# Optimization experiments

Hardware: AMD Instinct MI355X
Metric: run time of the kernel (lower is better)

Reference implementation:

```python
import jax, jax.numpy as jnp
import numpy as np

S, N, CM, CZ, H, D = 512, 768, 64, 128, 8, 32
EPS = 1e-5


def _layer_norm(x, w, b):
    mu = jnp.mean(x, axis=-1, keepdims=True)
    xc = x - mu
    var = jnp.mean(xc * xc, axis=-1, keepdims=True)
    return xc * jax.lax.rsqrt(var + EPS) * w + b


def setup_inputs() -> dict:
    key = jax.random.key(0)
    ks = jax.random.split(key, 6)
    scale_m = 1.0 / np.sqrt(CM)
    scale_z = 1.0 / np.sqrt(CZ)
    scale_o = 1.0 / np.sqrt(H * D)
    return {
        "m": jax.random.normal(ks[0], (1, S, N, CM), jnp.float32),
        "z": jax.random.normal(ks[1], (1, N, N, CZ), jnp.float32),
        "norm_m_w": jnp.ones((CM,), jnp.float32),
        "norm_m_b": jnp.zeros((CM,), jnp.float32),
        "norm_z_w": jnp.ones((CZ,), jnp.float32),
        "norm_z_b": jnp.zeros((CZ,), jnp.float32),
        "wm": jax.random.normal(ks[2], (CM, H * D), jnp.float32) * scale_m,
        "wg": jax.random.normal(ks[3], (CM, H * D), jnp.float32) * scale_m,
        "wz": jax.random.normal(ks[4], (CZ, H), jnp.float32) * scale_z,
        "wo": jax.random.normal(ks[5], (H * D, CM), jnp.float32) * scale_o,
    }


def reference(m, z, norm_m_w, norm_m_b, norm_z_w, norm_z_b, wm, wg, wz, wo):
    m0 = m[0]  # [S, N, CM]
    z0 = z[0]  # [N, N, CZ]
    mn = _layer_norm(m0, norm_m_w, norm_m_b)
    zn = _layer_norm(z0, norm_z_w, norm_z_b)
    # b[p,q,h]; original code softmaxes over the LAST axis of b'[h,p,q] (axis q)
    # but contracts as o[s,q] = sum_p w[p,q] v[s,p] (transpose_a matmul),
    # so softmax is over axis q = axis 1 of [p,q,h].
    b = jnp.einsum('pqc,ch->pqh', zn, wz)
    w = jax.nn.softmax(b, axis=1)  # normalized over q for each p (faithful to source)
    v = jnp.einsum('spc,ck->spk', mn, wm).reshape(S, N, H, D)
    g = jax.nn.sigmoid(jnp.einsum('spc,ck->spk', mn, wg)).reshape(S, N, H, D)
    o = jnp.einsum('pqh,sphd->sqhd', w, v) * g  # weighted average then gate
    out = jnp.einsum('sqhd,hdc->sqc', o, wo.reshape(H, D, CM))
    return out[None]  # [1, S, N, CM]
```

## Files before the change

kernel.cpp:

```cpp
#include <hip/hip_runtime.h>
#include <hip/hip_bf16.h>
#include <stdint.h>

#define S_DIM 512
#define N_DIM 768
#define CMd   64
#define CZd   128
#define Hd    8
#define Dd    32
#define HDd   256

typedef float          f32x4  __attribute__((ext_vector_type(4)));
typedef __bf16         bf16x8 __attribute__((ext_vector_type(8)));
typedef unsigned int   u32x4  __attribute__((ext_vector_type(4)));
typedef unsigned int   u32x2  __attribute__((ext_vector_type(2)));
typedef unsigned short u16x8  __attribute__((ext_vector_type(8)));

__device__ __forceinline__ unsigned short f2bf(float f) {
  __bf16 h = (__bf16)f;
  return __builtin_bit_cast(unsigned short, h);
}
__device__ __forceinline__ float bf2f(unsigned short u) {
  unsigned int x = ((unsigned int)u) << 16;
  return __builtin_bit_cast(float, x);
}
__device__ __forceinline__ float sigmoidf_(float x) {
  return 1.f / (1.f + __expf(-x));
}

typedef __attribute__((address_space(1))) const void cg_void;
typedef __attribute__((address_space(3))) void lds_void;
__device__ __forceinline__ void async16(const unsigned short* g, unsigned short* l) {
  __builtin_amdgcn_global_load_lds((cg_void*)g, (lds_void*)l, 16, 0, 0);
}

__global__ __launch_bounds__(256) void k0_prep(const float* __restrict__ wm,
                                               const float* __restrict__ wg,
                                               const float* __restrict__ wo,
                                               unsigned short* __restrict__ WBT,
                                               unsigned short* __restrict__ woT) {
  int t = blockIdx.x * 256 + threadIdx.x;
  if (t < 512 * 64) {
    int j = t >> 6, c = t & 63;
    float v = (j < 256) ? wm[c * 256 + j] : wg[c * 256 + (j - 256)];
    WBT[t] = f2bf(v);
  }
  if (t < 64 * 256) {
    int c = t >> 8, k = t & 255;
    woT[t] = f2bf(wo[k * 64 + c]);
  }
}

__global__ __launch_bounds__(256) void k1_zln_b(const float* __restrict__ z,
                                                const float* __restrict__ nzw,
                                                const float* __restrict__ nzb,
                                                const float* __restrict__ wz,
                                                float* __restrict__ b_e) {
  __shared__ float wzT[8][128];
  int t = threadIdx.x;
  for (int i = t; i < 1024; i += 256) {
    int h = i >> 7, c = i & 127;
    wzT[h][c] = wz[c * 8 + h];
  }
  __syncthreads();

  int lane = t & 63, w = t >> 6;
  int sub = lane & 7;
  int rloc = lane >> 3;
  int p = blockIdx.y;
  int q = blockIdx.x * 32 + w * 8 + rloc;

  const float* zr = z + ((size_t)p * N_DIM + q) * CZd + sub * 16;
  f32x4 v[4];
#pragma unroll
  for (int j = 0; j < 4; j++) v[j] = *(const f32x4*)(zr + 4 * j);

  float s1 = 0.f, s2 = 0.f;
#pragma unroll
  for (int j = 0; j < 4; j++)
#pragma unroll
    for (int e = 0; e < 4; e++) { float x = v[j][e]; s1 += x; s2 += x * x; }
  s1 += __shfl_xor(s1, 1); s2 += __shfl_xor(s2, 1);
  s1 += __shfl_xor(s1, 2); s2 += __shfl_xor(s2, 2);
  s1 += __shfl_xor(s1, 4); s2 += __shfl_xor(s2, 4);
  float mean = s1 * (1.f / 128.f);
  float var  = s2 * (1.f / 128.f) - mean * mean;
  float rstd = rsqrtf(var + 1e-5f);

  const float* wp = nzw + sub * 16;
  const float* bp = nzb + sub * 16;
  float zn[16];
#pragma unroll
  for (int j = 0; j < 4; j++) {
    f32x4 wv = *(const f32x4*)(wp + 4 * j);
    f32x4 bv = *(const f32x4*)(bp + 4 * j);
#pragma unroll
    for (int e = 0; e < 4; e++)
      zn[j * 4 + e] = (v[j][e] - mean) * rstd * wv[e] + bv[e];
  }

  float accb[8];
#pragma unroll
  for (int h = 0; h < 8; h++) {
    const f32x4* wr = (const f32x4*)&wzT[h][sub * 16];
    float a = 0.f;
#pragma unroll
    for (int j = 0; j < 4; j++) {
      f32x4 ww = wr[j];
#pragma unroll
      for (int e = 0; e < 4; e++) a += zn[j * 4 + e] * ww[e];
    }
    accb[h] = a;
  }
#pragma unroll
  for (int mask = 1; mask <= 4; mask <<= 1)
#pragma unroll
    for (int h = 0; h < 8; h++) accb[h] += __shfl_xor(accb[h], mask);

  float outv = accb[0];
#pragma unroll
  for (int h = 1; h < 8; h++) outv = (sub == h) ? accb[h] : outv;
  b_e[((size_t)p * 8 + sub) * 768 + q] = outv;
}

__global__ __launch_bounds__(256) void k1b_softmax(float* __restrict__ b_e,
                                                   float* __restrict__ invs) {
  int row = blockIdx.x;
  int t = threadIdx.x;
  float* base = b_e + (size_t)row * 768;
  float x0 = base[t], x1 = base[t + 256], x2 = base[t + 512];
  __shared__ float red[256];
  red[t] = fmaxf(x0, fmaxf(x1, x2));
  __syncthreads();
  for (int o = 128; o > 0; o >>= 1) {
    if (t < o) red[t] = fmaxf(red[t], red[t + o]);
    __syncthreads();
  }
  float M = red[0];
  __syncthreads();
  float e0 = __expf(x0 - M), e1 = __expf(x1 - M), e2 = __expf(x2 - M);
  base[t] = e0; base[t + 256] = e1; base[t + 512] = e2;
  red[t] = e0 + e1 + e2;
  __syncthreads();
  for (int o = 128; o > 0; o >>= 1) {
    if (t < o) red[t] += red[t + o];
    __syncthreads();
  }
  if (t == 0) invs[row] = 1.0f / red[0];
}

__global__ __launch_bounds__(256) void k1b2_transpose(const float* __restrict__ b_e,
                                                      const float* __restrict__ invs,
                                                      unsigned short* __restrict__ Aw) {
  int t = threadIdx.x;
  int q0 = blockIdx.x * 64, p0 = blockIdx.y * 64, h = blockIdx.z;
  __shared__ unsigned short T[64][65];
  int i = t >> 2, ch = t & 3;
  size_t rowid = (size_t)(p0 + i) * 8 + h;
  const float* src = b_e + rowid * 768 + q0 + ch * 16;
  float inv = invs[rowid];
#pragma unroll
  for (int jj = 0; jj < 16; jj += 4) {
    f32x4 v = *(const f32x4*)(src + jj);
#pragma unroll
    for (int e = 0; e < 4; e++) T[i][ch * 16 + jj + e] = f2bf(v[e] * inv);
  }
  __syncthreads();
  int j = i;
  unsigned short outv[16];
#pragma unroll
  for (int ii = 0; ii < 16; ii++) outv[ii] = T[ch * 16 + ii][j];
  int rx = (j & 7) << 3;
  unsigned short* dstrow = Aw + ((size_t)h * 768 + q0 + j) * 768 + p0;
  *(u32x4*)(dstrow + ((ch * 16) ^ rx))     = *(u32x4*)(outv);
  *(u32x4*)(dstrow + ((ch * 16 + 8) ^ rx)) = *(u32x4*)(outv + 8);
}

__global__ __launch_bounds__(256) void k2_mln_vg(const float* __restrict__ mp,
                                                 const float* __restrict__ nmw,
                                                 const float* __restrict__ nmb,
                                                 const unsigned short* __restrict__ WBT,
                                                 unsigned short* __restrict__ VT,
                                                 unsigned short* __restrict__ G) {
  __shared__ unsigned short WBs[512 * 64];
  __shared__ unsigned short As[64 * 64];
  int t = threadIdx.x;
  int p0 = blockIdx.x * 64, s = blockIdx.y;

#pragma unroll
  for (int it = 0; it < 16; it++) {
    int cid = t + it * 256;
    int row = cid >> 3, ch = cid & 7;
    u32x4 v = *(const u32x4*)(WBT + row * 64 + ch * 8);
    *(u32x4*)(WBs + row * 64 + ((ch * 8) ^ ((row & 7) << 3))) = v;
  }

  {
    int row = t >> 2, qt = t & 3;
    const float* mr = mp + ((size_t)s * N_DIM + p0 + row) * CMd + qt * 16;
    f32x4 v[4];
#pragma unroll
    for (int j = 0; j < 4; j++) v[j] = *(const f32x4*)(mr + 4 * j);
    float s1 = 0.f, s2 = 0.f;
#pragma unroll
    for (int j = 0; j < 4; j++)
#pragma unroll
      for (int e = 0; e < 4; e++) { float x = v[j][e]; s1 += x; s2 += x * x; }
    s1 += __shfl_xor(s1, 1); s2 += __shfl_xor(s2, 1);
    s1 += __shfl_xor(s1, 2); s2 += __shfl_xor(s2, 2);
    float mean = s1 * (1.f / 64.f);
    float var  = s2 * (1.f / 64.f) - mean * mean;
    float rstd = rsqrtf(var + 1e-5f);
    unsigned short o[16];
#pragma unroll
    for (int j = 0; j < 4; j++) {
      f32x4 wv = *(const f32x4*)(nmw + qt * 16 + 4 * j);
      f32x4 bv = *(const f32x4*)(nmb + qt * 16 + 4 * j);
#pragma unroll
      for (int e = 0; e < 4; e++)
        o[j * 4 + e] = f2bf((v[j][e] - mean) * rstd * wv[e] + bv[e]);
    }
    int k0 = qt * 16;
    *(u32x4*)(As + row * 64 + ((k0) ^ ((row & 7) << 3)))     = *(u32x4*)(o);
    *(u32x4*)(As + row * 64 + ((k0 + 8) ^ ((row & 7) << 3))) = *(u32x4*)(o + 8);
  }
  __syncthreads();

  int lane = t & 63, w = t >> 6;
  int n0 = w * 128;
  int lr = lane & 15, lg = lane >> 4, lk8 = lg * 8;
  f32x4 zero = {0.f, 0.f, 0.f, 0.f};
  f32x4 acc[4][8];
#pragma unroll
  for (int i = 0; i < 4; i++)
#pragma unroll
    for (int j = 0; j < 8; j++) acc[i][j] = zero;

#pragma unroll
  for (int kk = 0; kk < 2; kk++) {
    bf16x8 bfr[8];
#pragma unroll
    for (int nt = 0; nt < 8; nt++) {
      int r = n0 + nt * 16 + lr;
      bfr[nt] = *(const bf16x8*)(WBs + r * 64 + ((kk * 32 + lk8) ^ ((r & 7) << 3)));
    }
#pragma unroll
    for (int mt = 0; mt < 4; mt++) {
      int ar = mt * 16 + lr;
      bf16x8 a = *(const bf16x8*)(As + ar * 64 + ((kk * 32 + lk8) ^ ((ar & 7) << 3)));
#pragma unroll
      for (int nt = 0; nt < 8; nt++)
        acc[mt][nt] = __builtin_amdgcn_mfma_f32_16x16x32_bf16(a, bfr[nt], acc[mt][nt], 0, 0, 0);
    }
  }

  __syncthreads();

  {
    unsigned short* VL = WBs;
    if (w < 2) {
#pragma unroll
      for (int mt = 0; mt < 4; mt++)
#pragma unroll
        for (int nt = 0; nt < 8; nt++) {
          int j = n0 + nt * 16 + lr;
          int ploc = mt * 16 + lg * 4;
          unsigned short pk[4];
#pragma unroll
          for (int r = 0; r < 4; r++) pk[r] = f2bf(acc[mt][nt][r]);
          *(u32x2*)(VL + j * 72 + ploc) = *(u32x2*)pk;
        }
    }
    __syncthreads();
    int h = t >> 5, d = t & 31;
    unsigned short* dst = VT + ((size_t)h * 16384 + s * 32 + d) * 768 + p0;
    const unsigned short* src = VL + t * 72;
#pragma unroll
    for (int i = 0; i < 8; i++) {
      u32x4 v = *(const u32x4*)(src + i * 8);
      *(u32x4*)(dst + ((i ^ (d & 7)) * 8)) = v;
    }
  }
  __syncthreads();

  {
    unsigned short* GL = WBs;
    if (w >= 2) {
#pragma unroll
      for (int mt = 0; mt < 4; mt++)
#pragma unroll
        for (int nt = 0; nt < 8; nt++) {
          int jj = n0 - 256 + nt * 16 + lr;
          int ploc = mt * 16 + lg * 4;
#pragma unroll
          for (int r = 0; r < 4; r++)
            GL[(ploc + r) * 264 + jj] = f2bf(sigmoidf_(acc[mt][nt][r]));
        }
    }
    __syncthreads();
    int qrow = t >> 2, part = t & 3;
    unsigned short* dst = G + ((size_t)s * 768 + p0 + qrow) * 256 + part * 64;
    const unsigned short* src = GL + qrow * 264 + part * 64;
#pragma unroll
    for (int i = 0; i < 8; i++)
      *(u32x4*)(dst + i * 8) = *(const u32x4*)(src + i * 8);
  }
}

__global__ __launch_bounds__(256) void k3_gemm(const unsigned short* __restrict__ Aw,
                                               const unsigned short* __restrict__ VT,
                                               unsigned short* __restrict__ O) {
  __shared__ unsigned short Asl[128 * 64];
  __shared__ unsigned short Bsl[128 * 64];
  int t = threadIdx.x;
  int flat = blockIdx.x;
  int h = blockIdx.y;
  int f2 = (flat & 7) * 96 + (flat >> 3);
  int mt_b = f2 % 6, nt_b = f2 / 6;
  int q0 = mt_b * 128, n0 = nt_b * 128;

  const unsigned short* Ab = Aw + (size_t)h * 768 * 768 + (size_t)q0 * 768;
  const unsigned short* Bb = VT + (size_t)h * 16384 * 768 + (size_t)n0 * 768;

  int lane = t & 63, w = t >> 6;
  int wr = (w >> 1) * 64, wc = (w & 1) * 64;
  int lr = lane & 15;

  const unsigned short* gA = Ab + (size_t)(w * 32 + (lane >> 3)) * 768 + (lane & 7) * 8;
  const unsigned short* gB = Bb + (size_t)(w * 32 + (lane >> 3)) * 768 + (lane & 7) * 8;
  unsigned short* lA = Asl + w * 2048;
  unsigned short* lB = Bsl + w * 2048;

  f32x4 zero = {0.f, 0.f, 0.f, 0.f};
  f32x4 acc[4][4];
#pragma unroll
  for (int i = 0; i < 4; i++)
#pragma unroll
    for (int j = 0; j < 4; j++) acc[i][j] = zero;

  for (int kt = 0; kt < 12; kt++) {
    int ko = kt * 64;
#pragma unroll
    for (int i = 0; i < 4; i++) {
      async16(gA + (size_t)i * 8 * 768 + ko, lA + i * 512);
      async16(gB + (size_t)i * 8 * 768 + ko, lB + i * 512);
    }
    asm volatile("s_waitcnt vmcnt(0)" ::: "memory");
    __builtin_amdgcn_sched_barrier(0);
    __syncthreads();
#pragma unroll
    for (int kk = 0; kk < 2; kk++) {
      int kc = kk * 32 + (lane >> 4) * 8;
      bf16x8 afr[4], bfr[4];
#pragma unroll
      for (int i = 0; i < 4; i++) {
        int arr = wr + i * 16 + lr;
        int brr = wc + i * 16 + lr;
        afr[i] = *(const bf16x8*)(Asl + arr * 64 + (kc ^ ((arr & 7) << 3)));
        bfr[i] = *(const bf16x8*)(Bsl + brr * 64 + (kc ^ ((brr & 7) << 3)));
      }
#pragma unroll
      for (int mt = 0; mt < 4; mt++)
#pragma unroll
        for (int nt = 0; nt < 4; nt++)
          acc[mt][nt] = __builtin_amdgcn_mfma_f32_16x16x32_bf16(afr[mt], bfr[nt], acc[mt][nt], 0, 0, 0);
    }
    __syncthreads();
  }

#pragma unroll
  for (int mt = 0; mt < 4; mt++)
#pragma unroll
    for (int nt = 0; nt < 4; nt++) {
      int q = q0 + wr + mt * 16 + (lane >> 4) * 4;
      int n = n0 + wc + nt * 16 + lr;
      int s_ = n >> 5, d = n & 31;
      size_t ob = ((size_t)s_ * 768 + q) * 256 + h * 32 + d;
#pragma unroll
      for (int r = 0; r < 4; r++)
        O[ob + (size_t)r * 256] = f2bf(acc[mt][nt][r]);
    }
}

__global__ __launch_bounds__(256) void k4_out(const unsigned short* __restrict__ O,
                                              const unsigned short* __restrict__ G,
                                              const unsigned short* __restrict__ woT,
                                              float* __restrict__ out) {
  __shared__ unsigned short OGs[64 * 256];
  __shared__ unsigned short WOs[64 * 256];
  int t = threadIdx.x;
  int q0 = blockIdx.x * 64, s = blockIdx.y;

#pragma unroll
  for (int it = 0; it < 8; it++) {
    int cid = t + it * 256;
    int row = cid >> 5, ch = cid & 31;
    u32x4 v = *(const u32x4*)(woT + row * 256 + ch * 8);
    *(u32x4*)(WOs + row * 256 + ((ch * 8) ^ ((row & 7) << 3))) = v;
  }

  int i = t >> 2, c4 = t & 3;
  const unsigned short* Orow = O + ((size_t)s * 768 + q0 + i) * 256 + c4 * 64;
  const unsigned short* Grow = G + ((size_t)s * 768 + q0 + i) * 256 + c4 * 64;
#pragma unroll
  for (int jj = 0; jj < 8; jj++) {
    u16x8 ov = *(const u16x8*)(Orow + jj * 8);
    u16x8 gv = *(const u16x8*)(Grow + jj * 8);
    unsigned short pk[8];
#pragma unroll
    for (int e = 0; e < 8; e++) pk[e] = f2bf(bf2f(ov[e]) * bf2f(gv[e]));
    *(u32x4*)(OGs + i * 256 + ((c4 * 64 + jj * 8) ^ ((i & 7) << 3))) = *(u32x4*)pk;
  }
  __syncthreads();

  int lane = t & 63, w = t >> 6;
  int lr = lane & 15, lk8 = (lane >> 4) * 8;
  f32x4 zero = {0.f, 0.f, 0.f, 0.f};
  f32x4 acc[4];
#pragma unroll
  for (int nt = 0; nt < 4; nt++) acc[nt] = zero;

#pragma unroll
  for (int kk = 0; kk < 8; kk++) {
    int ar = w * 16 + lr;
    bf16x8 a = *(const bf16x8*)(OGs + ar * 256 + ((kk * 32 + lk8) ^ ((ar & 7) << 3)));
#pragma unroll
    for (int nt = 0; nt < 4; nt++) {
      int br = nt * 16 + lr;
      bf16x8 b = *(const bf16x8*)(WOs + br * 256 + ((kk * 32 + lk8) ^ ((br & 7) << 3)));
      acc[nt] = __builtin_amdgcn_mfma_f32_16x16x32_bf16(a, b, acc[nt], 0, 0, 0);
    }
  }

#pragma unroll
  for (int nt = 0; nt < 4; nt++) {
    int q = q0 + w * 16 + (lane >> 4) * 4;
    int c = nt * 16 + lr;
    float* dst = out + ((size_t)s * 768 + q) * 64 + c;
#pragma unroll
    for (int r = 0; r < 4; r++) dst[(size_t)r * 64] = acc[nt][r];
  }
}

extern "C" void kernel_launch(void* const* d_in, const int* in_sizes, int n_in,
                              void* d_out, int out_size, void* d_ws, size_t ws_size,
                              hipStream_t stream) {
  const float* m   = (const float*)d_in[0];
  const float* z   = (const float*)d_in[1];
  const float* nmw = (const float*)d_in[2];
  const float* nmb = (const float*)d_in[3];
  const float* nzw = (const float*)d_in[4];
  const float* nzb = (const float*)d_in[5];
  const float* wm  = (const float*)d_in[6];
  const float* wg  = (const float*)d_in[7];
  const float* wz  = (const float*)d_in[8];
  const float* wo  = (const float*)d_in[9];
  float* out = (float*)d_out;

  char* ws = (char*)d_ws;
  size_t off = 0;
  auto alloc = [&](size_t bytes) -> void* {
    void* p = ws + off;
    off += (bytes + 1023) & ~(size_t)1023;
    return p;
  };
  float*          b_e  = (float*)alloc((size_t)768 * 8 * 768 * 4);
  float*          invs = (float*)alloc((size_t)768 * 8 * 4);
  unsigned short* Awt  = (unsigned short*)alloc((size_t)8 * 768 * 768 * 2);
  unsigned short* WBT  = (unsigned short*)alloc((size_t)512 * 64 * 2);
  unsigned short* woT  = (unsigned short*)alloc((size_t)64 * 256 * 2);
  unsigned short* VT   = (unsigned short*)alloc((size_t)8 * 16384 * 768 * 2);
  unsigned short* G    = (unsigned short*)alloc((size_t)512 * 768 * 256 * 2);
  unsigned short* O    = (unsigned short*)alloc((size_t)512 * 768 * 256 * 2);
  if (ws_size < off) return;

  k0_prep<<<128, 256, 0, stream>>>(wm, wg, wo, WBT, woT);
  k1_zln_b<<<dim3(24, 768), 256, 0, stream>>>(z, nzw, nzb, wz, b_e);
  k1b_softmax<<<6144, 256, 0, stream>>>(b_e, invs);
  k1b2_transpose<<<dim3(12, 12, 8), 256, 0, stream>>>(b_e, invs, Awt);
  k2_mln_vg<<<dim3(12, 512), 256, 0, stream>>>(m, nmw, nmb, WBT, VT, G);
  k3_gemm<<<dim3(768, 8), 256, 0, stream>>>(Awt, VT, O);
  k4_out<<<dim3(12, 512), 256, 0, stream>>>(O, G, woT, out);
}
```

Baseline: 725.0 us.

## Split V/G projection across grid z and fuse gating into GEMM epilogue

The m-projection kernel is split into two grid halves, one computing V and one computing the sigmoid gate G. Weights are loaded straight from global memory into registers instead of a 64KB LDS copy, which cuts LDS use and allows a higher occupancy bound. The layer norm of m is now computed twice. The gate multiply moves from the output kernel into the k3 GEMM epilogue. That epilogue now reads G with a strided per-element pattern, while k4 no longer reads G at all.

```diff
diff --git a/kernel.cpp b/kernel.cpp
--- a/kernel.cpp
+++ b/kernel.cpp
@@ -176,24 +176,27 @@
   *(u32x4*)(dstrow + ((ch * 16 + 8) ^ rx)) = *(u32x4*)(outv + 8);
 }
 
-__global__ __launch_bounds__(256) void k2_mln_vg(const float* __restrict__ mp,
-                                                 const float* __restrict__ nmw,
-                                                 const float* __restrict__ nmb,
-                                                 const unsigned short* __restrict__ WBT,
-                                                 unsigned short* __restrict__ VT,
-                                                 unsigned short* __restrict__ G) {
-  __shared__ unsigned short WBs[512 * 64];
+__global__ __launch_bounds__(256, 3) void k2_mln_vg(const float* __restrict__ mp,
+                                                    const float* __restrict__ nmw,
+                                                    const float* __restrict__ nmb,
+                                                    const unsigned short* __restrict__ WBT,
+                                                    unsigned short* __restrict__ VT,
+                                                    unsigned short* __restrict__ G) {
   __shared__ unsigned short As[64 * 64];
-  int t = threadIdx.x;
-  int p0 = blockIdx.x * 64, s = blockIdx.y;
-
-#pragma unroll
-  for (int it = 0; it < 16; it++) {
-    int cid = t + it * 256;
-    int row = cid >> 3, ch = cid & 7;
-    u32x4 v = *(const u32x4*)(WBT + row * 64 + ch * 8);
-    *(u32x4*)(WBs + row * 64 + ((ch * 8) ^ ((row & 7) << 3))) = v;
-  }
+  __shared__ unsigned short TB[256 * 72];
+  int t = threadIdx.x;
+  int p0 = blockIdx.x * 64, s = blockIdx.y, nh = blockIdx.z;
+  int lane = t & 63, w = t >> 6;
+  int lr = lane & 15, lg = lane >> 4;
+
+  bf16x8 bfr[2][4];
+#pragma unroll
+  for (int kk = 0; kk < 2; kk++)
+#pragma unroll
+    for (int nt = 0; nt < 4; nt++) {
+      int j = nh * 256 + w * 64 + nt * 16 + lr;
+      bfr[kk][nt] = *(const bf16x8*)(WBT + j * 64 + kk * 32 + lg * 8);
+    }
 
   {
     int row = t >> 2, qt = t & 3;
@@ -226,81 +229,64 @@
   }
   __syncthreads();
 
-  int lane = t & 63, w = t >> 6;
-  int n0 = w * 128;
-  int lr = lane & 15, lg = lane >> 4, lk8 = lg * 8;
   f32x4 zero = {0.f, 0.f, 0.f, 0.f};
-  f32x4 acc[4][8];
+  f32x4 acc[4][4];
 #pragma unroll
   for (int i = 0; i < 4; i++)
 #pragma unroll
-    for (int j = 0; j < 8; j++) acc[i][j] = zero;
+    for (int j = 0; j < 4; j++) acc[i][j] = zero;
 
 #pragma unroll
   for (int kk = 0; kk < 2; kk++) {
-    bf16x8 bfr[8];
-#pragma unroll
-    for (int nt = 0; nt < 8; nt++) {
-      int r = n0 + nt * 16 + lr;
-      bfr[nt] = *(const bf16x8*)(WBs + r * 64 + ((kk * 32 + lk8) ^ ((r & 7) << 3)));
-    }
+    bf16x8 afr[4];
 #pragma unroll
     for (int mt = 0; mt < 4; mt++) {
       int ar = mt * 16 + lr;
-      bf16x8 a = *(const bf16x8*)(As + ar * 64 + ((kk * 32 + lk8) ^ ((ar & 7) << 3)));
-#pragma unroll
-      for (int nt = 0; nt < 8; nt++)
-        acc[mt][nt] = __builtin_amdgcn_mfma_f32_16x16x32_bf16(a, bfr[nt], acc[mt][nt], 0, 0, 0);
-    }
-  }
-
-  __syncthreads();
-
-  {
-    unsigned short* VL = WBs;
-    if (w < 2) {
-#pragma unroll
-      for (int mt = 0; mt < 4; mt++)
-#pragma unroll
-        for (int nt = 0; nt < 8; nt++) {
-          int j = n0 + nt * 16 + lr;
-          int ploc = mt * 16 + lg * 4;
-          unsigned short pk[4];
-#pragma unroll
-          for (int r = 0; r < 4; r++) pk[r] = f2bf(acc[mt][nt][r]);
-          *(u32x2*)(VL + j * 72 + ploc) = *(u32x2*)pk;
-        }
-    }
+      afr[mt] = *(const bf16x8*)(As + ar * 64 + ((kk * 32 + lg * 8) ^ ((ar & 7) << 3)));
+    }
+#pragma unroll
+    for (int mt = 0; mt < 4; mt++)
+#pragma unroll
+      for (int nt = 0; nt < 4; nt++)
+        acc[mt][nt] = __builtin_amdgcn_mfma_f32_16x16x32_bf16(afr[mt], bfr[kk][nt], acc[mt][nt], 0, 0, 0);
+  }
+
+  if (nh == 0) {
+#pragma unroll
+    for (int mt = 0; mt < 4; mt++)
+#pragma unroll
+      for (int nt = 0; nt < 4; nt++) {
+        int j = w * 64 + nt * 16 + lr;
+        int ploc = mt * 16 + lg * 4;
+        unsigned short pk[4];
+#pragma unroll
+        for (int r = 0; r < 4; r++) pk[r] = f2bf(acc[mt][nt][r]);
+        *(u32x2*)(TB + j * 72 + ploc) = *(u32x2*)pk;
+      }
     __syncthreads();
     int h = t >> 5, d = t & 31;
     unsigned short* dst = VT + ((size_t)h * 16384 + s * 32 + d) * 768 + p0;
-    const unsigned short* src = VL + t * 72;
+    const unsigned short* src = TB + t * 72;
 #pragma unroll
     for (int i = 0; i < 8; i++) {
       u32x4 v = *(const u32x4*)(src + i * 8);
       *(u32x4*)(dst + ((i ^ (d & 7)) * 8)) = v;
     }
-  }
-  __syncthreads();
-
-  {
-    unsigned short* GL = WBs;
-    if (w >= 2) {
-#pragma unroll
-      for (int mt = 0; mt < 4; mt++)
-#pragma unroll
-        for (int nt = 0; nt < 8; nt++) {
-          int jj = n0 - 256 + nt * 16 + lr;
-          int ploc = mt * 16 + lg * 4;
-#pragma unroll
-          for (int r = 0; r < 4; r++)
-            GL[(ploc + r) * 264 + jj] = f2bf(sigmoidf_(acc[mt][nt][r]));
-        }
-    }
+  } else {
+#pragma unroll
+    for (int mt = 0; mt < 4; mt++)
+#pragma unroll
+      for (int nt = 0; nt < 4; nt++) {
+        int jj = w * 64 + nt * 16 + lr;
+        int ploc = mt * 16 + lg * 4;
+#pragma unroll
+        for (int r = 0; r < 4; r++)
+          TB[(ploc + r) * 264 + jj] = f2bf(sigmoidf_(acc[mt][nt][r]));
+      }
     __syncthreads();
     int qrow = t >> 2, part = t & 3;
     unsigned short* dst = G + ((size_t)s * 768 + p0 + qrow) * 256 + part * 64;
-    const unsigned short* src = GL + qrow * 264 + part * 64;
+    const unsigned short* src = TB + qrow * 264 + part * 64;
 #pragma unroll
     for (int i = 0; i < 8; i++)
       *(u32x4*)(dst + i * 8) = *(const u32x4*)(src + i * 8);
@@ -309,6 +295,7 @@
 
 __global__ __launch_bounds__(256) void k3_gemm(const unsigned short* __restrict__ Aw,
                                                const unsigned short* __restrict__ VT,
+                                               const unsigned short* __restrict__ G,
                                                unsigned short* __restrict__ O) {
   __shared__ unsigned short Asl[128 * 64];
   __shared__ unsigned short Bsl[128 * 64];
@@ -377,13 +364,14 @@
       int s_ = n >> 5, d = n & 31;
       size_t ob = ((size_t)s_ * 768 + q) * 256 + h * 32 + d;
 #pragma unroll
-      for (int r = 0; r < 4; r++)
-        O[ob + (size_t)r * 256] = f2bf(acc[mt][nt][r]);
+      for (int r = 0; r < 4; r++) {
+        float gv = bf2f(G[ob + (size_t)r * 256]);
+        O[ob + (size_t)r * 256] = f2bf(acc[mt][nt][r] * gv);
+      }
     }
 }
 
 __global__ __launch_bounds__(256) void k4_out(const unsigned short* __restrict__ O,
-                                              const unsigned short* __restrict__ G,
                                               const unsigned short* __restrict__ woT,
                                               float* __restrict__ out) {
   __shared__ unsigned short OGs[64 * 256];
@@ -401,15 +389,10 @@
 
   int i = t >> 2, c4 = t & 3;
   const unsigned short* Orow = O + ((size_t)s * 768 + q0 + i) * 256 + c4 * 64;
-  const unsigned short* Grow = G + ((size_t)s * 768 + q0 + i) * 256 + c4 * 64;
 #pragma unroll
   for (int jj = 0; jj < 8; jj++) {
-    u16x8 ov = *(const u16x8*)(Orow + jj * 8);
-    u16x8 gv = *(const u16x8*)(Grow + jj * 8);
-    unsigned short pk[8];
-#pragma unroll
-    for (int e = 0; e < 8; e++) pk[e] = f2bf(bf2f(ov[e]) * bf2f(gv[e]));
-    *(u32x4*)(OGs + i * 256 + ((c4 * 64 + jj * 8) ^ ((i & 7) << 3))) = *(u32x4*)pk;
+    u32x4 ov = *(const u32x4*)(Orow + jj * 8);
+    *(u32x4*)(OGs + i * 256 + ((c4 * 64 + jj * 8) ^ ((i & 7) << 3))) = ov;
   }
   __syncthreads();
 
@@ -478,7 +461,7 @@
   k1_zln_b<<<dim3(24, 768), 256, 0, stream>>>(z, nzw, nzb, wz, b_e);
   k1b_softmax<<<6144, 256, 0, stream>>>(b_e, invs);
   k1b2_transpose<<<dim3(12, 12, 8), 256, 0, stream>>>(b_e, invs, Awt);
-  k2_mln_vg<<<dim3(12, 512), 256, 0, stream>>>(m, nmw, nmb, WBT, VT, G);
-  k3_gemm<<<dim3(768, 8), 256, 0, stream>>>(Awt, VT, O);
-  k4_out<<<dim3(12, 512), 256, 0, stream>>>(O, G, woT, out);
-}
+  k2_mln_vg<<<dim3(12, 512, 2), 256, 0, stream>>>(m, nmw, nmb, WBT, VT, G);
+  k3_gemm<<<dim3(768, 8), 256, 0, stream>>>(Awt, VT, G, O);
+  k4_out<<<dim3(12, 512), 256, 0, stream>>>(O, woT, out);
+}
```

New measurement: 678.3 us. 6.4% less time.
